# Performance work log

Measured on AMD Instinct MI355X. Metric: run time of the kernel, lower is better.

Reference implementation:

```python
import jax, jax.numpy as jnp
import numpy as np

INT_MIN, INT_MAX = -128.0, 127.0   # signed 8-bit weight range
UINT_MAX = 255.0                   # unsigned 8-bit activation range


def weight_quant(W):
    """Int8 per-tensor fixed-point (power-of-two scale from max-abs stats), STE."""
    max_abs = jax.lax.stop_gradient(jnp.max(jnp.abs(W)))
    # restrict threshold to power of two (ceil), scale = 2^e / 2^(bw-1)
    exp = jnp.ceil(jnp.log2(jnp.maximum(max_abs, 1e-12)))
    scale = jnp.exp2(exp) / 128.0
    q = jnp.clip(jnp.round(W / scale), INT_MIN, INT_MAX) * scale
    return W + jax.lax.stop_gradient(q - W)


def act_quant_relu(x, scale):
    """QuantReLU: relu then unsigned 8-bit quant-dequant with per-tensor scale, STE."""
    x = jax.nn.relu(x)
    s = jax.lax.stop_gradient(scale)
    q = jnp.clip(jnp.round(x / s), 0.0, UINT_MAX) * s
    return x + jax.lax.stop_gradient(q - x)


def setup_inputs() -> dict:
    key = jax.random.key(0)
    ks = jax.random.split(key, 9)
    B, D, U = 500000, 256, 64
    x = jax.random.normal(ks[0], (B, D), dtype=jnp.float32)
    W1 = jax.random.normal(ks[1], (U, D), dtype=jnp.float32) * (1.0 / np.sqrt(D))
    b1 = jax.random.normal(ks[2], (U,), dtype=jnp.float32) * 0.01
    W2 = jax.random.normal(ks[3], (U, U), dtype=jnp.float32) * (1.0 / np.sqrt(U))
    b2 = jax.random.normal(ks[4], (U,), dtype=jnp.float32) * 0.01
    Wout = jax.random.normal(ks[5], (1, U), dtype=jnp.float32) * (1.0 / np.sqrt(U))
    bout = jax.random.normal(ks[6], (1,), dtype=jnp.float32) * 0.01
    a1 = jax.random.uniform(ks[7], (), dtype=jnp.float32, minval=0.01, maxval=0.1)
    a2 = jax.random.uniform(ks[8], (), dtype=jnp.float32, minval=0.01, maxval=0.1)
    return {"x": x, "W1": W1, "b1": b1, "W2": W2, "b2": b2,
            "Wout": Wout, "bout": bout, "a1": a1, "a2": a2}


def reference(x, W1, b1, W2, b2, Wout, bout, a1, a2):
    # layer 1: quant-linear -> QuantReLU (dropout is identity at inference)
    h = x @ weight_quant(W1).T + b1
    h = act_quant_relu(h, a1)
    # layer 2
    h = h @ weight_quant(W2).T + b2
    h = act_quant_relu(h, a2)
    # output quant-linear (no activation quant)
    return h @ weight_quant(Wout).T + bout
```

## Files before the change

kernel.cpp:

```cpp
#include <hip/hip_runtime.h>

typedef __attribute__((ext_vector_type(8))) short s16x8;
typedef __attribute__((ext_vector_type(4))) float f32x4;

union FragU {
    unsigned int u[4];
    uint4 v;
    s16x8 s;
};

__device__ __forceinline__ float pow2_scale_inv(float ma, float& scale) {
    ma = fmaxf(ma, 1e-12f);
    unsigned u = __float_as_uint(ma);
    int E = (int)((u >> 23) & 255u);
    int ce = ((u & 0x7fffffu) == 0u) ? (E - 127) : (E - 126);
    int se = ce - 7;
    scale = __uint_as_float((unsigned)(se + 127) << 23);
    return __uint_as_float((unsigned)(127 - se) << 23);
}

__device__ __forceinline__ unsigned pack_hi16(unsigned u0, unsigned u1) {
    return __builtin_amdgcn_perm(u1, u0, 0x07060302u);
}

__device__ __forceinline__ float uni(float x) {
    return __uint_as_float((unsigned)__builtin_amdgcn_readfirstlane(__float_as_uint(x)));
}

__global__ __launch_bounds__(256, 1) void fused_kernel(
    const float* __restrict__ x,
    const float* __restrict__ W1,
    const float* __restrict__ b1,
    const float* __restrict__ W2,
    const float* __restrict__ b2,
    const float* __restrict__ Wo,
    const float* __restrict__ boutp,
    const float* __restrict__ a1p,
    const float* __restrict__ a2p,
    float* __restrict__ out,
    int ntiles) {

    __shared__ __align__(16) unsigned short w1f[16384];
    __shared__ __align__(16) unsigned short w2f[4096];
    __shared__ __align__(16) unsigned short stg[4][1024];
    __shared__ __align__(16) unsigned int   xbuf[4][4096];
    __shared__ float redm[12];

    const int t = threadIdx.x;
    const int lane = t & 63;
    const int wv = t >> 6;

    float m1 = 0.f, m2 = 0.f, mo = 0.f;
    #pragma unroll 4
    for (int k = 0; k < 16; ++k) {
        float4 v = *(const float4*)(W1 + 4 * (t + 256 * k));
        m1 = fmaxf(m1, fmaxf(fmaxf(fabsf(v.x), fabsf(v.y)),
                             fmaxf(fabsf(v.z), fabsf(v.w))));
    }
    #pragma unroll
    for (int k = 0; k < 4; ++k) {
        float4 v = *(const float4*)(W2 + 4 * (t + 256 * k));
        m2 = fmaxf(m2, fmaxf(fmaxf(fabsf(v.x), fabsf(v.y)),
                             fmaxf(fabsf(v.z), fabsf(v.w))));
    }
    if (t < 64) mo = fabsf(Wo[t]);

    #pragma unroll
    for (int m = 1; m < 64; m <<= 1) {
        m1 = fmaxf(m1, __shfl_xor(m1, m, 64));
        m2 = fmaxf(m2, __shfl_xor(m2, m, 64));
        mo = fmaxf(mo, __shfl_xor(mo, m, 64));
    }
    if (lane == 0) { redm[wv] = m1; redm[4 + wv] = m2; redm[8 + wv] = mo; }
    __syncthreads();
    m1 = fmaxf(fmaxf(redm[0], redm[1]), fmaxf(redm[2], redm[3]));
    m2 = fmaxf(fmaxf(redm[4], redm[5]), fmaxf(redm[6], redm[7]));
    mo = fmaxf(fmaxf(redm[8], redm[9]), fmaxf(redm[10], redm[11]));

    float s1v, s2v, sov;
    const float i1 = uni(pow2_scale_inv(m1, s1v));
    const float i2 = uni(pow2_scale_inv(m2, s2v));
    const float io = uni(pow2_scale_inv(mo, sov));
    const float s1 = uni(s1v);

    const float a1 = uni(a1p[0]), a2 = uni(a2p[0]);
    const double d1 = 1.0 / (double)a1;
    const float i1h = uni((float)d1), i1l = uni((float)(d1 - (double)(float)d1));
    const double d2 = 1.0 / (double)a2;
    const float i2h = uni((float)d2), i2l = uni((float)(d2 - (double)(float)d2));

    #pragma unroll 4
    for (int k = 0; k < 16; ++k) {
        const int i0 = 4 * (t + 256 * k);
        float4 v = *(const float4*)(W1 + i0);
        float q4[4] = {v.x, v.y, v.z, v.w};
        #pragma unroll
        for (int e = 0; e < 4; ++e) {
            const int i = i0 + e;
            float q = fminf(fmaxf(rintf(q4[e] * i1), -128.f), 127.f);
            const int u = i >> 8, kk = i & 255;
            const int c = u >> 4, ccb = u & 15, s = kk >> 5, gg = (kk >> 3) & 3, j = kk & 7;
            w1f[((s * 4 + c) * 64 + gg * 16 + ccb) * 8 + j] =
                (unsigned short)(__float_as_uint(q) >> 16);
        }
    }
    #pragma unroll
    for (int k = 0; k < 4; ++k) {
        const int i0 = 4 * (t + 256 * k);
        float4 v = *(const float4*)(W2 + i0);
        float q4[4] = {v.x, v.y, v.z, v.w};
        #pragma unroll
        for (int e = 0; e < 4; ++e) {
            const int i = i0 + e;
            float q = fminf(fmaxf(rintf(q4[e] * i2), -128.f), 127.f);
            const int vv = i >> 6, kk = i & 63;
            const int c = vv >> 4, ccb = vv & 15, s = kk >> 5, gg = (kk >> 3) & 3, j = kk & 7;
            w2f[((s * 4 + c) * 64 + gg * 16 + ccb) * 8 + j] =
                (unsigned short)(__float_as_uint(q) >> 16);
        }
    }
    __syncthreads();

    const float boutv = uni(boutp[0]);
    const float c21 = uni(a1 * s2v);
    const float c3  = uni(a2 * sov);

    const int cc = lane & 15;
    const int g  = lane >> 4;

    float b1c[4], b2c[4], wqc[4];
    #pragma unroll
    for (int c = 0; c < 4; ++c) {
        b1c[c] = b1[c * 16 + cc];
        b2c[c] = b2[c * 16 + cc];
        wqc[c] = fminf(fmaxf(rintf(Wo[c * 16 + cc] * io), -128.f), 127.f);
    }

    unsigned short* st = stg[wv];

    const char* xbc = (const char*)xbuf[wv];
    const char* xr0 = xbc + cc * 1024 + (((2 * g + 0 + cc) & 7) << 4);
    const char* xr1 = xbc + cc * 1024 + (((2 * g + 1 + cc) & 7) << 4);
    const int lreg = (lane >> 3) << 7;

    const int b = blockIdx.x;
    const int nb = gridDim.x;
    const int pb = (nb & 7) ? b : ((b & 7) * (nb >> 3) + (b >> 3));
    const int S = (int)(((long long)pb * ntiles) / nb);
    const int E = (int)(((long long)(pb + 1) * ntiles) / nb);
    const int t0 = S + wv;

    if (t0 < E) {
        const char* gs = (const char*)(x + (size_t)t0 * 4096);
        #pragma unroll
        for (int r = 0; r < 16; ++r) {
            const int so = lreg + (((lane - r) & 7) << 4);
            __builtin_amdgcn_global_load_lds(
                (const unsigned int*)(gs + r * 1024 + so),
                &xbuf[wv][r * 256], 16, 0, 0);
        }
    }
    asm volatile("s_waitcnt vmcnt(0)" ::: "memory");
    __builtin_amdgcn_sched_barrier(0);

    for (int tile = t0; tile < E; tile += 4) {
        const int nt = tile + 4;
        const bool hasnext = nt < E;

        f32x4 acc[4];
        #pragma unroll
        for (int c = 0; c < 4; ++c) acc[c] = (f32x4){0.f, 0.f, 0.f, 0.f};

        #pragma unroll
        for (int ks = 0; ks < 8; ++ks) {
            const float4 A = *(const float4*)(xr0 + ks * 128);
            const float4 B = *(const float4*)(xr1 + ks * 128);

            float f[8] = {A.x, A.y, A.z, A.w, B.x, B.y, B.z, B.w};
            FragU hi, lo, lo2;
            #pragma unroll
            for (int p = 0; p < 4; ++p) {
                const float f0 = f[2 * p], f1 = f[2 * p + 1];
                const unsigned u0 = __float_as_uint(f0), u1 = __float_as_uint(f1);
                hi.u[p] = pack_hi16(u0, u1);
                const float r0 = f0 - __uint_as_float(u0 & 0xffff0000u);
                const float r1 = f1 - __uint_as_float(u1 & 0xffff0000u);
                const unsigned v0 = __float_as_uint(r0), v1 = __float_as_uint(r1);
                lo.u[p] = pack_hi16(v0, v1);
                const float q0 = r0 - __uint_as_float(v0 & 0xffff0000u);
                const float q1 = r1 - __uint_as_float(v1 & 0xffff0000u);
                lo2.u[p] = pack_hi16(__float_as_uint(q0), __float_as_uint(q1));
            }
            #pragma unroll
            for (int c = 0; c < 4; ++c) {
                FragU bb;
                bb.v = *(const uint4*)&w1f[((ks * 4 + c) * 64 + lane) * 8];
                acc[c] = __builtin_amdgcn_mfma_f32_16x16x32_bf16(hi.s,  bb.s, acc[c], 0, 0, 0);
                acc[c] = __builtin_amdgcn_mfma_f32_16x16x32_bf16(lo.s,  bb.s, acc[c], 0, 0, 0);
                acc[c] = __builtin_amdgcn_mfma_f32_16x16x32_bf16(lo2.s, bb.s, acc[c], 0, 0, 0);
            }
        }

        asm volatile("s_waitcnt lgkmcnt(0)" ::: "memory");
        __builtin_amdgcn_sched_barrier(0);
        if (hasnext) {
            const char* gs = (const char*)(x + (size_t)nt * 4096);
            #pragma unroll
            for (int r = 0; r < 16; ++r) {
                const int so = lreg + (((lane - r) & 7) << 4);
                __builtin_amdgcn_global_load_lds(
                    (const unsigned int*)(gs + r * 1024 + so),
                    &xbuf[wv][r * 256], 16, 0, 0);
            }
        }
        __builtin_amdgcn_sched_barrier(0);

        #pragma unroll
        for (int c = 0; c < 4; ++c) {
            #pragma unroll
            for (int j = 0; j < 4; ++j) {
                float h = fmaf(acc[c][j], s1, b1c[c]);
                h = fmaxf(h, 0.f);
                float n = rintf(fmaf(h, i1l, h * i1h));
                n = fminf(n, 255.f);
                const int r = g * 4 + j;
                const int u = c * 16 + cc;
                const int pos = ((u >> 5) * 64 + ((u >> 3) & 3) * 16 + r) * 8 + (u & 7);
                st[pos] = (unsigned short)(__float_as_uint(n) >> 16);
            }
        }
        asm volatile("s_waitcnt lgkmcnt(0)" ::: "memory");

        s16x8 afrag[2];
        #pragma unroll
        for (int s = 0; s < 2; ++s) {
            FragU a;
            a.v = *(const uint4*)&st[(s * 64 + lane) * 8];
            afrag[s] = a.s;
        }

        f32x4 acc2[4];
        #pragma unroll
        for (int c = 0; c < 4; ++c) acc2[c] = (f32x4){0.f, 0.f, 0.f, 0.f};
        #pragma unroll
        for (int s = 0; s < 2; ++s) {
            #pragma unroll
            for (int c = 0; c < 4; ++c) {
                FragU bb;
                bb.v = *(const uint4*)&w2f[((s * 4 + c) * 64 + lane) * 8];
                acc2[c] = __builtin_amdgcn_mfma_f32_16x16x32_bf16(afrag[s], bb.s, acc2[c], 0, 0, 0);
            }
        }

        float psum[4] = {0.f, 0.f, 0.f, 0.f};
        #pragma unroll
        for (int c = 0; c < 4; ++c) {
            #pragma unroll
            for (int j = 0; j < 4; ++j) {
                float h = fmaf(acc2[c][j], c21, b2c[c]);
                h = fmaxf(h, 0.f);
                float n = rintf(fmaf(h, i2l, h * i2h));
                n = fminf(n, 255.f);
                psum[j] = fmaf(n, wqc[c], psum[j]);
            }
        }
        #pragma unroll
        for (int j = 0; j < 4; ++j) {
            #pragma unroll
            for (int mask = 1; mask < 16; mask <<= 1)
                psum[j] += __shfl_xor(psum[j], mask, 16);
        }

        if (cc == 0) {
            float4 o;
            o.x = fmaf(psum[0], c3, boutv);
            o.y = fmaf(psum[1], c3, boutv);
            o.z = fmaf(psum[2], c3, boutv);
            o.w = fmaf(psum[3], c3, boutv);
            *(float4*)(out + (size_t)tile * 16 + g * 4) = o;
        }

        asm volatile("s_waitcnt vmcnt(1)" ::: "memory");
        __builtin_amdgcn_sched_barrier(0);
    }
}

extern "C" void kernel_launch(void* const* d_in, const int* in_sizes, int n_in,
                              void* d_out, int out_size, void* d_ws, size_t ws_size,
                              hipStream_t stream) {
    const float* x    = (const float*)d_in[0];
    const float* W1   = (const float*)d_in[1];
    const float* b1   = (const float*)d_in[2];
    const float* W2   = (const float*)d_in[3];
    const float* b2   = (const float*)d_in[4];
    const float* Wout = (const float*)d_in[5];
    const float* bout = (const float*)d_in[6];
    const float* a1   = (const float*)d_in[7];
    const float* a2   = (const float*)d_in[8];
    float* out = (float*)d_out;

    const int rows = in_sizes[0] / 256;
    const int ntiles = rows / 16;

    int blocks = 256;
    if (blocks * 4 > ntiles) blocks = (ntiles + 3) / 4;
    fused_kernel<<<blocks, 256, 0, stream>>>(x, W1, b1, W2, b2, Wout, bout,
                                             a1, a2, out, ntiles);
}
```

Measured before the change: 130.2 us.

## Split each tile's output columns across waves and run two blocks per CU

```diff
diff --git a/kernel.cpp b/kernel.cpp
--- a/kernel.cpp
+++ b/kernel.cpp
@@ -27,7 +27,14 @@
     return __uint_as_float((unsigned)__builtin_amdgcn_readfirstlane(__float_as_uint(x)));
 }
 
-__global__ __launch_bounds__(256, 1) void fused_kernel(
+__device__ __forceinline__ void lds_barrier() {
+    asm volatile("s_waitcnt lgkmcnt(0)" ::: "memory");
+    __builtin_amdgcn_sched_barrier(0);
+    __builtin_amdgcn_s_barrier();
+    __builtin_amdgcn_sched_barrier(0);
+}
+
+__global__ __launch_bounds__(256, 2) void fused_kernel(
     const float* __restrict__ x,
     const float* __restrict__ W1,
     const float* __restrict__ b1,
@@ -42,8 +49,9 @@
 
     __shared__ __align__(16) unsigned short w1f[16384];
     __shared__ __align__(16) unsigned short w2f[4096];
-    __shared__ __align__(16) unsigned short stg[4][1024];
-    __shared__ __align__(16) unsigned int   xbuf[4][4096];
+    __shared__ __align__(16) unsigned short stg[1024];
+    __shared__ __align__(16) float partial[64];
+    __shared__ __align__(16) unsigned int xb[2][4096];
     __shared__ float redm[12];
 
     const int t = threadIdx.x;
@@ -128,19 +136,12 @@
     const int cc = lane & 15;
     const int g  = lane >> 4;
 
-    float b1c[4], b2c[4], wqc[4];
-    #pragma unroll
-    for (int c = 0; c < 4; ++c) {
-        b1c[c] = b1[c * 16 + cc];
-        b2c[c] = b2[c * 16 + cc];
-        wqc[c] = fminf(fmaxf(rintf(Wo[c * 16 + cc] * io), -128.f), 127.f);
-    }
-
-    unsigned short* st = stg[wv];
-
-    const char* xbc = (const char*)xbuf[wv];
-    const char* xr0 = xbc + cc * 1024 + (((2 * g + 0 + cc) & 7) << 4);
-    const char* xr1 = xbc + cc * 1024 + (((2 * g + 1 + cc) & 7) << 4);
+    const float b1c = b1[wv * 16 + cc];
+    const float b2c = b2[wv * 16 + cc];
+    const float wqc = fminf(fmaxf(rintf(Wo[wv * 16 + cc] * io), -128.f), 127.f);
+
+    const int xo0 = cc * 1024 + (((2 * g + 0 + cc) & 7) << 4);
+    const int xo1 = cc * 1024 + (((2 * g + 1 + cc) & 7) << 4);
     const int lreg = (lane >> 3) << 7;
 
     const int b = blockIdx.x;
@@ -148,33 +149,44 @@
     const int pb = (nb & 7) ? b : ((b & 7) * (nb >> 3) + (b >> 3));
     const int S = (int)(((long long)pb * ntiles) / nb);
     const int E = (int)(((long long)(pb + 1) * ntiles) / nb);
-    const int t0 = S + wv;
-
-    if (t0 < E) {
-        const char* gs = (const char*)(x + (size_t)t0 * 4096);
-        #pragma unroll
-        for (int r = 0; r < 16; ++r) {
+
+    if (S < E) {
+        const char* gs = (const char*)(x + (size_t)S * 4096);
+        #pragma unroll
+        for (int r4 = 0; r4 < 4; ++r4) {
+            const int r = wv * 4 + r4;
             const int so = lreg + (((lane - r) & 7) << 4);
             __builtin_amdgcn_global_load_lds(
-                (const unsigned int*)(gs + r * 1024 + so),
-                &xbuf[wv][r * 256], 16, 0, 0);
+                (const unsigned int*)(gs + r * 1024 + so), &xb[0][r * 256], 16, 0, 0);
         }
     }
     asm volatile("s_waitcnt vmcnt(0)" ::: "memory");
     __builtin_amdgcn_sched_barrier(0);
-
-    for (int tile = t0; tile < E; tile += 4) {
-        const int nt = tile + 4;
-        const bool hasnext = nt < E;
-
-        f32x4 acc[4];
-        #pragma unroll
-        for (int c = 0; c < 4; ++c) acc[c] = (f32x4){0.f, 0.f, 0.f, 0.f};
+    __builtin_amdgcn_s_barrier();
+    __builtin_amdgcn_sched_barrier(0);
+
+    for (int tile = S; tile < E; ++tile) {
+        const int cur = (tile - S) & 1;
+
+        if (tile + 1 < E) {
+            const char* gs = (const char*)(x + (size_t)(tile + 1) * 4096);
+            #pragma unroll
+            for (int r4 = 0; r4 < 4; ++r4) {
+                const int r = wv * 4 + r4;
+                const int so = lreg + (((lane - r) & 7) << 4);
+                __builtin_amdgcn_global_load_lds(
+                    (const unsigned int*)(gs + r * 1024 + so),
+                    &xb[cur ^ 1][r * 256], 16, 0, 0);
+            }
+        }
+
+        const char* xbc = (const char*)xb[cur];
+        f32x4 acc = (f32x4){0.f, 0.f, 0.f, 0.f};
 
         #pragma unroll
         for (int ks = 0; ks < 8; ++ks) {
-            const float4 A = *(const float4*)(xr0 + ks * 128);
-            const float4 B = *(const float4*)(xr1 + ks * 128);
+            const float4 A = *(const float4*)(xbc + xo0 + ks * 128);
+            const float4 B = *(const float4*)(xbc + xo1 + ks * 128);
 
             float f[8] = {A.x, A.y, A.z, A.w, B.x, B.y, B.z, B.w};
             FragU hi, lo, lo2;
@@ -191,78 +203,50 @@
                 const float q1 = r1 - __uint_as_float(v1 & 0xffff0000u);
                 lo2.u[p] = pack_hi16(__float_as_uint(q0), __float_as_uint(q1));
             }
-            #pragma unroll
-            for (int c = 0; c < 4; ++c) {
-                FragU bb;
-                bb.v = *(const uint4*)&w1f[((ks * 4 + c) * 64 + lane) * 8];
-                acc[c] = __builtin_amdgcn_mfma_f32_16x16x32_bf16(hi.s,  bb.s, acc[c], 0, 0, 0);
-                acc[c] = __builtin_amdgcn_mfma_f32_16x16x32_bf16(lo.s,  bb.s, acc[c], 0, 0, 0);
-                acc[c] = __builtin_amdgcn_mfma_f32_16x16x32_bf16(lo2.s, bb.s, acc[c], 0, 0, 0);
-            }
-        }
-
-        asm volatile("s_waitcnt lgkmcnt(0)" ::: "memory");
-        __builtin_amdgcn_sched_barrier(0);
-        if (hasnext) {
-            const char* gs = (const char*)(x + (size_t)nt * 4096);
-            #pragma unroll
-            for (int r = 0; r < 16; ++r) {
-                const int so = lreg + (((lane - r) & 7) << 4);
-                __builtin_amdgcn_global_load_lds(
-                    (const unsigned int*)(gs + r * 1024 + so),
-                    &xbuf[wv][r * 256], 16, 0, 0);
-            }
-        }
-        __builtin_amdgcn_sched_barrier(0);
-
-        #pragma unroll
-        for (int c = 0; c < 4; ++c) {
-            #pragma unroll
-            for (int j = 0; j < 4; ++j) {
-                float h = fmaf(acc[c][j], s1, b1c[c]);
-                h = fmaxf(h, 0.f);
-                float n = rintf(fmaf(h, i1l, h * i1h));
-                n = fminf(n, 255.f);
-                const int r = g * 4 + j;
-                const int u = c * 16 + cc;
-                const int pos = ((u >> 5) * 64 + ((u >> 3) & 3) * 16 + r) * 8 + (u & 7);
-                st[pos] = (unsigned short)(__float_as_uint(n) >> 16);
-            }
-        }
-        asm volatile("s_waitcnt lgkmcnt(0)" ::: "memory");
+            FragU bb;
+            bb.v = *(const uint4*)&w1f[((ks * 4 + wv) * 64 + lane) * 8];
+            acc = __builtin_amdgcn_mfma_f32_16x16x32_bf16(hi.s,  bb.s, acc, 0, 0, 0);
+            acc = __builtin_amdgcn_mfma_f32_16x16x32_bf16(lo.s,  bb.s, acc, 0, 0, 0);
+            acc = __builtin_amdgcn_mfma_f32_16x16x32_bf16(lo2.s, bb.s, acc, 0, 0, 0);
+        }
+
+        #pragma unroll
+        for (int j = 0; j < 4; ++j) {
+            float h = fmaf(acc[j], s1, b1c);
+            h = fmaxf(h, 0.f);
+            float n = rintf(fmaf(h, i1l, h * i1h));
+            n = fminf(n, 255.f);
+            const int r = g * 4 + j;
+            const int u = wv * 16 + cc;
+            const int pos = ((u >> 5) * 64 + ((u >> 3) & 3) * 16 + r) * 8 + (u & 7);
+            stg[pos] = (unsigned short)(__float_as_uint(n) >> 16);
+        }
+        lds_barrier();
 
         s16x8 afrag[2];
         #pragma unroll
         for (int s = 0; s < 2; ++s) {
             FragU a;
-            a.v = *(const uint4*)&st[(s * 64 + lane) * 8];
+            a.v = *(const uint4*)&stg[(s * 64 + lane) * 8];
             afrag[s] = a.s;
         }
 
-        f32x4 acc2[4];
-        #pragma unroll
-        for (int c = 0; c < 4; ++c) acc2[c] = (f32x4){0.f, 0.f, 0.f, 0.f};
+        f32x4 acc2 = (f32x4){0.f, 0.f, 0.f, 0.f};
         #pragma unroll
         for (int s = 0; s < 2; ++s) {
-            #pragma unroll
-            for (int c = 0; c < 4; ++c) {
-                FragU bb;
-                bb.v = *(const uint4*)&w2f[((s * 4 + c) * 64 + lane) * 8];
-                acc2[c] = __builtin_amdgcn_mfma_f32_16x16x32_bf16(afrag[s], bb.s, acc2[c], 0, 0, 0);
-            }
-        }
-
-        float psum[4] = {0.f, 0.f, 0.f, 0.f};
-        #pragma unroll
-        for (int c = 0; c < 4; ++c) {
-            #pragma unroll
-            for (int j = 0; j < 4; ++j) {
-                float h = fmaf(acc2[c][j], c21, b2c[c]);
-                h = fmaxf(h, 0.f);
-                float n = rintf(fmaf(h, i2l, h * i2h));
-                n = fminf(n, 255.f);
-                psum[j] = fmaf(n, wqc[c], psum[j]);
-            }
+            FragU bb;
+            bb.v = *(const uint4*)&w2f[((s * 4 + wv) * 64 + lane) * 8];
+            acc2 = __builtin_amdgcn_mfma_f32_16x16x32_bf16(afrag[s], bb.s, acc2, 0, 0, 0);
+        }
+
+        float psum[4];
+        #pragma unroll
+        for (int j = 0; j < 4; ++j) {
+            float h = fmaf(acc2[j], c21, b2c);
+            h = fmaxf(h, 0.f);
+            float n = rintf(fmaf(h, i2l, h * i2h));
+            n = fminf(n, 255.f);
+            psum[j] = n * wqc;
         }
         #pragma unroll
         for (int j = 0; j < 4; ++j) {
@@ -270,18 +254,25 @@
             for (int mask = 1; mask < 16; mask <<= 1)
                 psum[j] += __shfl_xor(psum[j], mask, 16);
         }
-
         if (cc == 0) {
-            float4 o;
-            o.x = fmaf(psum[0], c3, boutv);
-            o.y = fmaf(psum[1], c3, boutv);
-            o.z = fmaf(psum[2], c3, boutv);
-            o.w = fmaf(psum[3], c3, boutv);
-            *(float4*)(out + (size_t)tile * 16 + g * 4) = o;
-        }
-
-        asm volatile("s_waitcnt vmcnt(1)" ::: "memory");
+            float4 pw = {psum[0], psum[1], psum[2], psum[3]};
+            *(float4*)&partial[wv * 16 + g * 4] = pw;
+        }
+        lds_barrier();
+
+        float oval = 0.f;
+        if (wv == 0 && lane < 16) {
+            oval = (partial[lane] + partial[16 + lane]) +
+                   (partial[32 + lane] + partial[48 + lane]);
+            oval = fmaf(oval, c3, boutv);
+        }
+
+        asm volatile("s_waitcnt vmcnt(0)" ::: "memory");
         __builtin_amdgcn_sched_barrier(0);
+        __builtin_amdgcn_s_barrier();
+        __builtin_amdgcn_sched_barrier(0);
+
+        if (wv == 0 && lane < 16) out[(size_t)tile * 16 + lane] = oval;
     }
 }
 
@@ -302,8 +293,8 @@
     const int rows = in_sizes[0] / 256;
     const int ntiles = rows / 16;
 
-    int blocks = 256;
-    if (blocks * 4 > ntiles) blocks = (ntiles + 3) / 4;
+    int blocks = 512;
+    if (blocks > ntiles) blocks = ntiles;
     fused_kernel<<<blocks, 256, 0, stream>>>(x, W1, b1, W2, b2, Wout, bout,
                                              a1, a2, out, ntiles);
 }
```

Result: slower. 159.4 us (+22.4%).
